# Optimization experiments

Hardware: AMD Instinct MI355X
Metric: run time of the kernel (lower is better)

## Reference

```python
import math
import jax, jax.numpy as jnp
import numpy as np

B, S, D, H = 2, 2048, 2048, 16
HD = D // H  # head_dim = 128, rotary_dim = HD (full rotation)
ROPE_BASE = 10000.0


def setup_inputs() -> dict:
    key = jax.random.key(0)
    k0, k1, k2 = jax.random.split(key, 3)
    return {
        "x": jax.random.normal(k0, (B, S, D), dtype=jnp.float32),
        "Wqkv": jax.random.normal(k1, (D, 3 * D), dtype=jnp.float32) * 0.02,
        "bqkv": jnp.zeros((3 * D,), dtype=jnp.float32),
        "Wout": jax.random.normal(k2, (D, D), dtype=jnp.float32) * 0.02,
        "bout": jnp.zeros((D,), dtype=jnp.float32),
    }


def _rope_cos_sin(seqlen, dim):
    # flash-attn RotaryEmbedding: inv_freq over even indices, outer with positions
    inv_freq = 1.0 / (ROPE_BASE ** (jnp.arange(0, dim, 2, dtype=jnp.float32) / dim))
    t = jnp.arange(seqlen, dtype=jnp.float32)
    freqs = jnp.outer(t, inv_freq)  # (S, dim/2)
    return jnp.cos(freqs), jnp.sin(freqs)


def reference(x, Wqkv, bqkv, Wout, bout):
    b, s, d = x.shape
    hd = d // H
    # fused QKV projection -> (B, S, 3, H, HD)
    qkv = (x @ Wqkv + bqkv).reshape(b, s, 3, H, hd)
    q, k, v = qkv[:, :, 0], qkv[:, :, 1], qkv[:, :, 2]  # (B,S,H,HD)

    cos, sin = _rope_cos_sin(s, hd)
    c = cos[:, None, :]  # (S,1,HD/2) broadcast over heads
    si = sin[:, None, :]

    def rot(t):
        # split-half rotary (as in apply_rotary_emb_qkv), computed in fp32
        t1, t2 = jnp.split(t.astype(jnp.float32), 2, axis=-1)
        return jnp.concatenate([t1 * c - t2 * si, t1 * si + t2 * c], axis=-1).astype(x.dtype)

    q = rot(q)
    k = rot(k)

    scale = 1.0 / math.sqrt(hd)
    scores = jnp.einsum("bthd,bshd->bhts", q, k * scale)  # (B,H,S,S)
    causal_mask = jnp.triu(jnp.full((s, s), -10000.0, dtype=scores.dtype), 1)
    attn = jax.nn.softmax(scores + causal_mask, axis=-1)
    ctx = jnp.einsum("bhts,bshd->bthd", attn, v).reshape(b, s, d)
    return ctx @ Wout + bout
```

## Files before the change

### kernel.cpp

```cpp
#include <hip/hip_runtime.h>
#include <hip/hip_bf16.h>

typedef __attribute__((ext_vector_type(4))) float fx4;
typedef __attribute__((ext_vector_type(8))) short bx8;
typedef __hip_bfloat16 bf16;

#define GLD16(dst, src)                                                        \
  __builtin_amdgcn_global_load_lds(                                            \
      (__attribute__((address_space(1))) void*)(src),                          \
      (__attribute__((address_space(3))) void*)(dst), 16, 0, 0)

__device__ inline float bf2f(short s_) {
  unsigned int u = ((unsigned int)(unsigned short)s_) << 16;
  float f;
  __builtin_memcpy(&f, &u, 4);
  return f;
}
__device__ inline short f2bf(float f) {
  __hip_bfloat16 h = __float2bfloat16(f);
  short r;
  __builtin_memcpy(&r, &h, 2);
  return r;
}

__global__ __launch_bounds__(256) void k_cast(const float* __restrict__ in,
                                              bf16* __restrict__ out, int n4) {
  int i = blockIdx.x * 256 + threadIdx.x;
  if (i >= n4) return;
  float4 v = reinterpret_cast<const float4*>(in)[i];
  bf16 t[4] = {__float2bfloat16(v.x), __float2bfloat16(v.y),
               __float2bfloat16(v.z), __float2bfloat16(v.w)};
  reinterpret_cast<ushort4*>(out)[i] = *reinterpret_cast<ushort4*>(t);
}

__global__ void k_tcast(const float* __restrict__ in, bf16* __restrict__ out,
                        int R, int C) {
  __shared__ float tile[32][33];
  int c0 = blockIdx.x * 32, r0 = blockIdx.y * 32;
  int tx = threadIdx.x, ty = threadIdx.y;
#pragma unroll
  for (int j = 0; j < 4; ++j)
    tile[ty + j * 8][tx] = in[(size_t)(r0 + ty + j * 8) * C + c0 + tx];
  __syncthreads();
#pragma unroll
  for (int j = 0; j < 4; ++j)
    out[(size_t)(c0 + ty + j * 8) * R + r0 + tx] =
        __float2bfloat16(tile[tx][ty + j * 8]);
}

__global__ __launch_bounds__(256) void k_ropetab(float* __restrict__ cosT,
                                                 float* __restrict__ sinT) {
  int idx = blockIdx.x * 256 + threadIdx.x;
  int t = idx >> 6, i = idx & 63;
  float inv = expf(-logf(10000.0f) * (float)i * (1.0f / 64.0f));
  float fr = (float)t * inv;
  cosT[idx] = cosf(fr);
  sinT[idx] = sinf(fr);
}

__global__ __launch_bounds__(256) void k_rope(bf16* __restrict__ qkv,
                                              const float* __restrict__ cosT,
                                              const float* __restrict__ sinT) {
  int t = blockIdx.x * 256 + threadIdx.x;
  int d0 = (t & 7) * 8;
  int qk = (t >> 3) & 1;
  int h = (t >> 4) & 15;
  int s = (t >> 8) & 2047;
  int b = (t >> 19) & 1;
  bf16* base = qkv + (size_t)(b * 2048 + s) * 6144 + qk * 2048 + h * 128;
  bx8 lo = *(const bx8*)(base + d0);
  bx8 hi = *(const bx8*)(base + 64 + d0);
  float4 ca = *(const float4*)&cosT[s * 64 + d0];
  float4 cb = *(const float4*)&cosT[s * 64 + d0 + 4];
  float4 sa = *(const float4*)&sinT[s * 64 + d0];
  float4 sb = *(const float4*)&sinT[s * 64 + d0 + 4];
  float c[8] = {ca.x, ca.y, ca.z, ca.w, cb.x, cb.y, cb.z, cb.w};
  float si[8] = {sa.x, sa.y, sa.z, sa.w, sb.x, sb.y, sb.z, sb.w};
  bx8 olo, ohi;
#pragma unroll
  for (int e = 0; e < 8; ++e) {
    float t1 = bf2f(lo[e]), t2 = bf2f(hi[e]);
    olo[e] = f2bf(t1 * c[e] - t2 * si[e]);
    ohi[e] = f2bf(t1 * si[e] + t2 * c[e]);
  }
  *(bx8*)(base + d0) = olo;
  *(bx8*)(base + 64 + d0) = ohi;
}

__global__ void k_vtrans(const bf16* __restrict__ qkv, bf16* __restrict__ vT) {
  __shared__ bf16 tile[32][33];
  int s0 = blockIdx.x * 32, d0 = blockIdx.y * 32, bh = blockIdx.z;
  int b = bh >> 4, h = bh & 15;
  int tx = threadIdx.x, ty = threadIdx.y;
#pragma unroll
  for (int j = 0; j < 4; ++j)
    tile[ty + j * 8][tx] =
        qkv[(size_t)(b * 2048 + s0 + ty + j * 8) * 6144 + 4096 + h * 128 + d0 + tx];
  __syncthreads();
#pragma unroll
  for (int j = 0; j < 4; ++j)
    vT[(size_t)(bh * 128 + d0 + ty + j * 8) * 2048 + s0 + tx] = tile[tx][ty + j * 8];
}

__global__ __launch_bounds__(512, 4) void k_gemm256(
    const bf16* __restrict__ A, const bf16* __restrict__ BT,
    const float* __restrict__ bias, bf16* __restrict__ C, int M, int N, int K,
    int NBX) {
  __shared__ __align__(16) bf16 As[2][256 * 32];
  __shared__ __align__(16) bf16 Bs[2][128 * 32];
  const int tid = threadIdx.x;
  const int lane = tid & 63, wid = tid >> 6;
  const int lr = lane & 15, lg = lane >> 4;
  const int wr = wid >> 1, wc = wid & 1;
  const int nwg = gridDim.x, bid = blockIdx.x;
  const int swz = (bid & 7) * (nwg >> 3) + (bid >> 3);
  const int mb = swz / NBX, nb = swz - mb * NBX;
  const int m0 = mb * 256, n0 = nb * 128;
  const int NT = K >> 5;

  fx4 acc[4][4];
#pragma unroll
  for (int m = 0; m < 4; ++m)
#pragma unroll
    for (int n = 0; n < 4; ++n) acc[m][n] = (fx4)(0.0f);

  auto SA = [&](int buf, int t) {
#pragma unroll
    for (int q = 0; q < 2; ++q) {
      const int L = q * 512 + tid;
      const int row = L >> 2, u = L & 3;
      GLD16(&As[buf][L * 8],
            A + (size_t)(m0 + row) * K + t * 32 + ((u ^ ((row >> 1) & 3)) * 8));
    }
  };
  auto SB = [&](int buf, int t) {
    const int L = tid;
    const int row = L >> 2, u = L & 3;
    GLD16(&Bs[buf][L * 8],
          BT + (size_t)(n0 + row) * K + t * 32 + ((u ^ ((row >> 1) & 3)) * 8));
  };

  SA(0, 0); SB(0, 0);
  asm volatile("s_waitcnt vmcnt(0)" ::: "memory");
  __builtin_amdgcn_s_barrier();

  for (int t = 0; t < NT; ++t) {
    const int buf = t & 1;
    if (t + 1 < NT) { SA(buf ^ 1, t + 1); SB(buf ^ 1, t + 1); }
    bx8 af[4], bfr[4];
#pragma unroll
    for (int m = 0; m < 4; ++m) {
      const int r = wr * 64 + m * 16 + lr;
      af[m] = *(const bx8*)&As[buf][r * 32 + ((lg ^ ((r >> 1) & 3)) * 8)];
    }
#pragma unroll
    for (int n = 0; n < 4; ++n) {
      const int r = wc * 64 + n * 16 + lr;
      bfr[n] = *(const bx8*)&Bs[buf][r * 32 + ((lg ^ ((r >> 1) & 3)) * 8)];
    }
    asm volatile("s_waitcnt lgkmcnt(0)" ::: "memory");
    __builtin_amdgcn_sched_barrier(0);
    __builtin_amdgcn_s_setprio(1);
#pragma unroll
    for (int m = 0; m < 4; ++m)
#pragma unroll
      for (int n = 0; n < 4; ++n)
        acc[m][n] =
            __builtin_amdgcn_mfma_f32_16x16x32_bf16(af[m], bfr[n], acc[m][n], 0, 0, 0);
    __builtin_amdgcn_s_setprio(0);
    asm volatile("s_waitcnt vmcnt(0)" ::: "memory");
    __builtin_amdgcn_s_barrier();
  }

  float bv[4];
#pragma unroll
  for (int n = 0; n < 4; ++n) bv[n] = bias[n0 + wc * 64 + n * 16 + lr];
#pragma unroll
  for (int m = 0; m < 4; ++m)
#pragma unroll
    for (int n = 0; n < 4; ++n) {
      const int col = n0 + wc * 64 + n * 16 + lr;
#pragma unroll
      for (int j = 0; j < 4; ++j) {
        const int row = m0 + wr * 64 + m * 16 + lg * 4 + j;
        C[(size_t)row * N + col] = __float2bfloat16(acc[m][n][j] + bv[n]);
      }
    }
}

__global__ __launch_bounds__(256) void k_gemm_bt(
    const bf16* __restrict__ A, const bf16* __restrict__ BT,
    const float* __restrict__ bias, void* __restrict__ Cp, int M, int N, int K,
    int out_bf16) {
  __shared__ __align__(16) bf16 As[128 * 64];
  __shared__ __align__(16) bf16 Bs[128 * 64];
  const int tid = threadIdx.x;
  const int m0 = blockIdx.y * 128, n0 = blockIdx.x * 128;
  const int lane = tid & 63, w = tid >> 6;
  const int lr = lane & 15, lg = lane >> 4;
  const int wr = w >> 1, wc = w & 1;

  fx4 acc[4][4];
#pragma unroll
  for (int m = 0; m < 4; ++m)
#pragma unroll
    for (int n = 0; n < 4; ++n) acc[m][n] = (fx4)(0.0f);

  for (int kt = 0; kt < K; kt += 64) {
#pragma unroll
    for (int q = 0; q < 4; ++q) {
      const int slot = q * 256 + tid;
      const int row = slot >> 3, u = slot & 7;
      const int us = (u ^ (row & 7)) * 8;
      GLD16(&As[slot * 8], A + (size_t)(m0 + row) * K + kt + us);
      GLD16(&Bs[slot * 8], BT + (size_t)(n0 + row) * K + kt + us);
    }
    __syncthreads();
#pragma unroll
    for (int ks = 0; ks < 2; ++ks) {
      bx8 af[4], bf[4];
#pragma unroll
      for (int m = 0; m < 4; ++m) {
        const int r = wr * 64 + m * 16 + lr;
        const int u = ((ks * 4 + lg) ^ (lr & 7)) * 8;
        af[m] = *(const bx8*)&As[r * 64 + u];
      }
#pragma unroll
      for (int n = 0; n < 4; ++n) {
        const int r = wc * 64 + n * 16 + lr;
        const int u = ((ks * 4 + lg) ^ (lr & 7)) * 8;
        bf[n] = *(const bx8*)&Bs[r * 64 + u];
      }
#pragma unroll
      for (int m = 0; m < 4; ++m)
#pragma unroll
        for (int n = 0; n < 4; ++n)
          acc[m][n] =
              __builtin_amdgcn_mfma_f32_16x16x32_bf16(af[m], bf[n], acc[m][n], 0, 0, 0);
    }
    __syncthreads();
  }

  float bv[4];
#pragma unroll
  for (int n = 0; n < 4; ++n) bv[n] = bias[n0 + wc * 64 + n * 16 + lr];

#pragma unroll
  for (int m = 0; m < 4; ++m)
#pragma unroll
    for (int n = 0; n < 4; ++n) {
      const int col = n0 + wc * 64 + n * 16 + lr;
#pragma unroll
      for (int j = 0; j < 4; ++j) {
        const int row = m0 + wr * 64 + m * 16 + lg * 4 + j;
        const float v = acc[m][n][j] + bv[n];
        if (out_bf16)
          ((bf16*)Cp)[(size_t)row * N + col] = __float2bfloat16(v);
        else
          ((float*)Cp)[(size_t)row * N + col] = v;
      }
    }
}

#define ATT_SL2E 0.12751740f

__global__ __launch_bounds__(256, 2) void k_attn2(
    const bf16* __restrict__ qkv, const bf16* __restrict__ vT,
    bf16* __restrict__ ctx, float* __restrict__ O0, float* __restrict__ O1,
    float* __restrict__ l0, float* __restrict__ l1) {
  __shared__ __align__(16) bf16 Ks[2][128 * 128];
  __shared__ __align__(16) bf16 Ps[4][32 * 64];
  const int tid = threadIdx.x;
  const int lane = tid & 63, w = tid >> 6;
  const int lr = lane & 15, lg = lane >> 4;
  const int bid = blockIdx.x;
  const int u = bid >> 5, bh = bid & 31;
  const int b = bh >> 4, h = bh & 15;
  int qt, t0, t1;
  if (u < 8) {
    qt = 8 + u; t0 = 0; t1 = 8;
  } else if (u < 16) {
    qt = 23 - u; t0 = 8; t1 = qt + 1;
  } else {
    qt = 23 - u; t0 = 0; t1 = qt + 1;
  }
  const int single = (u >= 16);
  const int nt = t1 - t0;

  const bf16* kbase = qkv + (size_t)b * 2048 * 6144 + 2048 + h * 128;
  const bf16* vbase = vT + (size_t)(b * 16 + h) * 128 * 2048;

  auto STAGE = [&](int bufi, int kt) {
    const int kv0 = kt * 128;
#pragma unroll
    for (int q = 0; q < 8; ++q) {
      const int slot = q * 256 + tid;
      const int row = slot >> 4, uu = slot & 15;
      GLD16(&Ks[bufi][slot * 8],
            kbase + (size_t)(kv0 + row) * 6144 + ((uu ^ (row & 15)) * 8));
    }
  };

  const bf16* qbase =
      qkv + (size_t)(b * 2048 + qt * 128 + w * 32) * 6144 + h * 128;
  bx8 qf[2][4];
#pragma unroll
  for (int m = 0; m < 2; ++m)
#pragma unroll
    for (int ks = 0; ks < 4; ++ks)
      qf[m][ks] = *(const bx8*)(qbase + (size_t)(m * 16 + lr) * 6144 + ks * 32 + lg * 8);

  bx8 vones;
#pragma unroll
  for (int e = 0; e < 8; ++e) vones[e] = (short)0x3F80;

  fx4 oacc[2][8], lacc[2];
#pragma unroll
  for (int m = 0; m < 2; ++m) {
    lacc[m] = (fx4)(0.0f);
#pragma unroll
    for (int d = 0; d < 8; ++d) oacc[m][d] = (fx4)(0.0f);
  }

  const int qrow0 = qt * 128 + w * 32;

  STAGE(0, t0);
  for (int i = 0; i < nt; ++i) {
    const int kt = t0 + i;
    const int cur = i & 1;
    if (i + 1 < nt) {
      STAGE(cur ^ 1, kt + 1);
      asm volatile("s_waitcnt vmcnt(8)" ::: "memory");
    } else {
      asm volatile("s_waitcnt vmcnt(0)" ::: "memory");
    }
    __builtin_amdgcn_s_barrier();
    asm volatile("" ::: "memory");

#pragma unroll
    for (int h2 = 0; h2 < 2; ++h2) {
      const int kv0 = kt * 128 + h2 * 64;
      if (kv0 > qrow0 + 31) continue;

      fx4 sacc[2][4];
#pragma unroll
      for (int n = 0; n < 4; ++n) {
        sacc[0][n] = (fx4)(0.0f);
        sacc[1][n] = (fx4)(0.0f);
      }
      __builtin_amdgcn_s_setprio(1);
#pragma unroll
      for (int n = 0; n < 4; ++n) {
        const int r = h2 * 64 + n * 16 + lr;
#pragma unroll
        for (int ks = 0; ks < 4; ++ks) {
          const bx8 kf = *(const bx8*)&Ks[cur][r * 128 + (((ks * 4 + lg) ^ lr) * 8)];
          sacc[0][n] =
              __builtin_amdgcn_mfma_f32_16x16x32_bf16(qf[0][ks], kf, sacc[0][n], 0, 0, 0);
          sacc[1][n] =
              __builtin_amdgcn_mfma_f32_16x16x32_bf16(qf[1][ks], kf, sacc[1][n], 0, 0, 0);
        }
      }
      __builtin_amdgcn_s_setprio(0);

      const bool needmask = (kv0 + 63) > qrow0;
#pragma unroll
      for (int n = 0; n < 4; ++n) {
        const int kvi = kv0 + n * 16 + lr;
#pragma unroll
        for (int m = 0; m < 2; ++m)
#pragma unroll
          for (int j = 0; j < 4; ++j) {
            float v = sacc[m][n][j] * ATT_SL2E;
            if (needmask) {
              const int qi = qrow0 + m * 16 + lg * 4 + j;
              if (kvi > qi) v = -200.0f;
            }
            const float p = exp2f(fminf(v, 60.0f));
            const int r = m * 16 + lg * 4 + j, c = n * 16 + lr;
            const int c2 = (c & 7) | (((c >> 3) ^ (r & 7)) << 3);
            Ps[w][r * 64 + c2] = __float2bfloat16(p);
          }
      }

      __builtin_amdgcn_s_setprio(1);
#pragma unroll
      for (int ks2 = 0; ks2 < 2; ++ks2) {
        const int uu = ((ks2 * 4 + lg) ^ (lr & 7)) * 8;
        const bx8 pf0 = *(const bx8*)&Ps[w][(0 * 16 + lr) * 64 + uu];
        const bx8 pf1 = *(const bx8*)&Ps[w][(1 * 16 + lr) * 64 + uu];
        lacc[0] = __builtin_amdgcn_mfma_f32_16x16x32_bf16(pf0, vones, lacc[0], 0, 0, 0);
        lacc[1] = __builtin_amdgcn_mfma_f32_16x16x32_bf16(pf1, vones, lacc[1], 0, 0, 0);
#pragma unroll
        for (int dn = 0; dn < 8; ++dn) {
          const bx8 vf = *(const bx8*)(vbase + (size_t)(dn * 16 + lr) * 2048 + kv0 +
                                       ks2 * 32 + lg * 8);
          oacc[0][dn] =
              __builtin_amdgcn_mfma_f32_16x16x32_bf16(pf0, vf, oacc[0][dn], 0, 0, 0);
          oacc[1][dn] =
              __builtin_amdgcn_mfma_f32_16x16x32_bf16(pf1, vf, oacc[1][dn], 0, 0, 0);
        }
      }
      __builtin_amdgcn_s_setprio(0);
    }
    __builtin_amdgcn_s_barrier();
    asm volatile("" ::: "memory");
  }

  if (single) {
    float rl[2][4];
#pragma unroll
    for (int m = 0; m < 2; ++m)
#pragma unroll
      for (int j = 0; j < 4; ++j) rl[m][j] = 1.0f / lacc[m][j];
#pragma unroll
    for (int m = 0; m < 2; ++m)
#pragma unroll
      for (int dn = 0; dn < 8; ++dn)
#pragma unroll
        for (int j = 0; j < 4; ++j) {
          const int row = qt * 128 + w * 32 + m * 16 + lg * 4 + j;
          ctx[(size_t)(b * 2048 + row) * 2048 + h * 128 + dn * 16 + lr] =
              __float2bfloat16(oacc[m][dn][j] * rl[m][j]);
        }
  } else {
    float* Op = (u < 8) ? O0 : O1;
    float* lp = (u < 8) ? l0 : l1;
    float* obase =
        Op + (((size_t)(b * 16 + h)) * 1024 + (qt * 128 - 1024 + w * 32)) * 128;
#pragma unroll
    for (int m = 0; m < 2; ++m)
#pragma unroll
      for (int dn = 0; dn < 8; ++dn)
#pragma unroll
        for (int j = 0; j < 4; ++j)
          obase[(m * 16 + lg * 4 + j) * 128 + dn * 16 + lr] = oacc[m][dn][j];
    if (lr == 0) {
      float* lbase =
          lp + ((size_t)(b * 16 + h)) * 1024 + (qt * 128 - 1024 + w * 32);
#pragma unroll
      for (int m = 0; m < 2; ++m)
#pragma unroll
        for (int j = 0; j < 4; ++j) lbase[m * 16 + lg * 4 + j] = lacc[m][j];
    }
  }
}

__global__ __launch_bounds__(256) void k_comb(const float* __restrict__ O0,
                                              const float* __restrict__ O1,
                                              const float* __restrict__ l0,
                                              const float* __restrict__ l1,
                                              bf16* __restrict__ ctx) {
  const int idx = blockIdx.x * 256 + threadIdx.x;
  const size_t base = (size_t)idx * 8;
  const size_t rowi = base >> 7;
  const float rl = 1.0f / (l0[rowi] + l1[rowi]);
  const float4 a0 = *(const float4*)&O0[base];
  const float4 b0 = *(const float4*)&O0[base + 4];
  const float4 a1 = *(const float4*)&O1[base];
  const float4 b1 = *(const float4*)&O1[base + 4];
  const int d = (int)(base & 127);
  const int s = (int)(rowi & 1023);
  const int bh = (int)(rowi >> 10);
  const int b = bh >> 4, h = bh & 15;
  bf16 o[8] = {__float2bfloat16((a0.x + a1.x) * rl), __float2bfloat16((a0.y + a1.y) * rl),
               __float2bfloat16((a0.z + a1.z) * rl), __float2bfloat16((a0.w + a1.w) * rl),
               __float2bfloat16((b0.x + b1.x) * rl), __float2bfloat16((b0.y + b1.y) * rl),
               __float2bfloat16((b0.z + b1.z) * rl), __float2bfloat16((b0.w + b1.w) * rl)};
  bf16* p = ctx + (size_t)(b * 2048 + 1024 + s) * 2048 + h * 128 + d;
  *(ushort4*)p = *(ushort4*)o;
  *(ushort4*)(p + 4) = *(ushort4*)(o + 4);
}

extern "C" void kernel_launch(void* const* d_in, const int* in_sizes, int n_in,
                              void* d_out, int out_size, void* d_ws, size_t ws_size,
                              hipStream_t stream) {
  const float* x = (const float*)d_in[0];
  const float* Wqkv = (const float*)d_in[1];
  const float* bqkv = (const float*)d_in[2];
  const float* Wout = (const float*)d_in[3];
  const float* bout = (const float*)d_in[4];
  float* out = (float*)d_out;

  char* ws = (char*)d_ws;
  bf16* xb    = (bf16*)(ws + 0);
  bf16* wqkvT = (bf16*)(ws + 16777216);
  bf16* woutT = (bf16*)(ws + 41943040);
  bf16* qkvb  = (bf16*)(ws + 50331648);
  bf16* vTb   = (bf16*)(ws + 100663296);
  bf16* ctxb  = (bf16*)(ws + 117440512);
  float* cosT = (float*)(ws + 134217728);
  float* sinT = (float*)(ws + 134742016);
  float* O0 = (float*)(ws + 0);
  float* O1 = (float*)(ws + 16777216);
  float* l0 = (float*)(ws + 33554432);
  float* l1 = (float*)(ws + 33685504);

  k_cast<<<8192, 256, 0, stream>>>(x, xb, 2097152);
  k_tcast<<<dim3(192, 64), dim3(32, 8), 0, stream>>>(Wqkv, wqkvT, 2048, 6144);
  k_tcast<<<dim3(64, 64), dim3(32, 8), 0, stream>>>(Wout, woutT, 2048, 2048);
  k_ropetab<<<512, 256, 0, stream>>>(cosT, sinT);
  k_gemm256<<<768, 512, 0, stream>>>(xb, wqkvT, bqkv, qkvb, 4096, 6144, 2048, 48);
  k_rope<<<4096, 256, 0, stream>>>(qkvb, cosT, sinT);
  k_vtrans<<<dim3(64, 4, 32), dim3(32, 8), 0, stream>>>(qkvb, vTb);
  k_attn2<<<768, 256, 0, stream>>>(qkvb, vTb, ctxb, O0, O1, l0, l1);
  k_comb<<<2048, 256, 0, stream>>>(O0, O1, l0, l1, ctxb);
  k_gemm_bt<<<dim3(16, 32), 256, 0, stream>>>(ctxb, woutT, bout, out, 4096, 2048,
                                              2048, 0);
}
```

Baseline: 336.7 us.

## Reuse pipelined 256x128 GEMM for output projection and restructure its wait/barrier schedule

Generalizes the 256x128 double-buffered GEMM kernel to write either bf16 or fp32 and uses it for the output projection, replacing the older 128x128 kernel that had no prefetch overlap. The main loop now issues the next tile's async loads first, then waits only for the current tile with a partial vmcnt before the barrier. Loads for the next tile can therefore overlap compute instead of being drained at the end of each iteration. The output GEMM launches only 256 workgroups, which may underfill the GPU, and vmcnt(3) assumes exactly three loads are issued per thread per tile.

```diff
diff --git a/kernel.cpp b/kernel.cpp
--- a/kernel.cpp
+++ b/kernel.cpp
@@ -104,8 +104,8 @@
 
 __global__ __launch_bounds__(512, 4) void k_gemm256(
     const bf16* __restrict__ A, const bf16* __restrict__ BT,
-    const float* __restrict__ bias, bf16* __restrict__ C, int M, int N, int K,
-    int NBX) {
+    const float* __restrict__ bias, void* __restrict__ Cp, int M, int N, int K,
+    int NBX, int out_bf16) {
   __shared__ __align__(16) bf16 As[2][256 * 32];
   __shared__ __align__(16) bf16 Bs[2][128 * 32];
   const int tid = threadIdx.x;
@@ -141,12 +141,17 @@
   };
 
   SA(0, 0); SB(0, 0);
-  asm volatile("s_waitcnt vmcnt(0)" ::: "memory");
-  __builtin_amdgcn_s_barrier();
 
   for (int t = 0; t < NT; ++t) {
     const int buf = t & 1;
-    if (t + 1 < NT) { SA(buf ^ 1, t + 1); SB(buf ^ 1, t + 1); }
+    if (t + 1 < NT) {
+      SA(buf ^ 1, t + 1); SB(buf ^ 1, t + 1);
+      asm volatile("s_waitcnt vmcnt(3)" ::: "memory");
+    } else {
+      asm volatile("s_waitcnt vmcnt(0)" ::: "memory");
+    }
+    __builtin_amdgcn_s_barrier();
+
     bx8 af[4], bfr[4];
 #pragma unroll
     for (int m = 0; m < 4; ++m) {
@@ -168,83 +173,12 @@
         acc[m][n] =
             __builtin_amdgcn_mfma_f32_16x16x32_bf16(af[m], bfr[n], acc[m][n], 0, 0, 0);
     __builtin_amdgcn_s_setprio(0);
-    asm volatile("s_waitcnt vmcnt(0)" ::: "memory");
     __builtin_amdgcn_s_barrier();
   }
 
   float bv[4];
 #pragma unroll
   for (int n = 0; n < 4; ++n) bv[n] = bias[n0 + wc * 64 + n * 16 + lr];
-#pragma unroll
-  for (int m = 0; m < 4; ++m)
-#pragma unroll
-    for (int n = 0; n < 4; ++n) {
-      const int col = n0 + wc * 64 + n * 16 + lr;
-#pragma unroll
-      for (int j = 0; j < 4; ++j) {
-        const int row = m0 + wr * 64 + m * 16 + lg * 4 + j;
-        C[(size_t)row * N + col] = __float2bfloat16(acc[m][n][j] + bv[n]);
-      }
-    }
-}
-
-__global__ __launch_bounds__(256) void k_gemm_bt(
-    const bf16* __restrict__ A, const bf16* __restrict__ BT,
-    const float* __restrict__ bias, void* __restrict__ Cp, int M, int N, int K,
-    int out_bf16) {
-  __shared__ __align__(16) bf16 As[128 * 64];
-  __shared__ __align__(16) bf16 Bs[128 * 64];
-  const int tid = threadIdx.x;
-  const int m0 = blockIdx.y * 128, n0 = blockIdx.x * 128;
-  const int lane = tid & 63, w = tid >> 6;
-  const int lr = lane & 15, lg = lane >> 4;
-  const int wr = w >> 1, wc = w & 1;
-
-  fx4 acc[4][4];
-#pragma unroll
-  for (int m = 0; m < 4; ++m)
-#pragma unroll
-    for (int n = 0; n < 4; ++n) acc[m][n] = (fx4)(0.0f);
-
-  for (int kt = 0; kt < K; kt += 64) {
-#pragma unroll
-    for (int q = 0; q < 4; ++q) {
-      const int slot = q * 256 + tid;
-      const int row = slot >> 3, u = slot & 7;
-      const int us = (u ^ (row & 7)) * 8;
-      GLD16(&As[slot * 8], A + (size_t)(m0 + row) * K + kt + us);
-      GLD16(&Bs[slot * 8], BT + (size_t)(n0 + row) * K + kt + us);
-    }
-    __syncthreads();
-#pragma unroll
-    for (int ks = 0; ks < 2; ++ks) {
-      bx8 af[4], bf[4];
-#pragma unroll
-      for (int m = 0; m < 4; ++m) {
-        const int r = wr * 64 + m * 16 + lr;
-        const int u = ((ks * 4 + lg) ^ (lr & 7)) * 8;
-        af[m] = *(const bx8*)&As[r * 64 + u];
-      }
-#pragma unroll
-      for (int n = 0; n < 4; ++n) {
-        const int r = wc * 64 + n * 16 + lr;
-        const int u = ((ks * 4 + lg) ^ (lr & 7)) * 8;
-        bf[n] = *(const bx8*)&Bs[r * 64 + u];
-      }
-#pragma unroll
-      for (int m = 0; m < 4; ++m)
-#pragma unroll
-        for (int n = 0; n < 4; ++n)
-          acc[m][n] =
-              __builtin_amdgcn_mfma_f32_16x16x32_bf16(af[m], bf[n], acc[m][n], 0, 0, 0);
-    }
-    __syncthreads();
-  }
-
-  float bv[4];
-#pragma unroll
-  for (int n = 0; n < 4; ++n) bv[n] = bias[n0 + wc * 64 + n * 16 + lr];
-
 #pragma unroll
   for (int m = 0; m < 4; ++m)
 #pragma unroll
@@ -500,11 +434,10 @@
   k_tcast<<<dim3(192, 64), dim3(32, 8), 0, stream>>>(Wqkv, wqkvT, 2048, 6144);
   k_tcast<<<dim3(64, 64), dim3(32, 8), 0, stream>>>(Wout, woutT, 2048, 2048);
   k_ropetab<<<512, 256, 0, stream>>>(cosT, sinT);
-  k_gemm256<<<768, 512, 0, stream>>>(xb, wqkvT, bqkv, qkvb, 4096, 6144, 2048, 48);
+  k_gemm256<<<768, 512, 0, stream>>>(xb, wqkvT, bqkv, qkvb, 4096, 6144, 2048, 48, 1);
   k_rope<<<4096, 256, 0, stream>>>(qkvb, cosT, sinT);
   k_vtrans<<<dim3(64, 4, 32), dim3(32, 8), 0, stream>>>(qkvb, vTb);
   k_attn2<<<768, 256, 0, stream>>>(qkvb, vTb, ctxb, O0, O1, l0, l1);
   k_comb<<<2048, 256, 0, stream>>>(O0, O1, l0, l1, ctxb);
-  k_gemm_bt<<<dim3(16, 32), 256, 0, stream>>>(ctxb, woutT, bout, out, 4096, 2048,
-                                              2048, 0);
-}
+  k_gemm256<<<256, 512, 0, stream>>>(ctxb, woutT, bout, out, 4096, 2048, 2048, 16, 0);
+}
```

Result: slower. 347.7 us (+3.3%).
